# Kernel optimization log

Measured on AMD Instinct MI355X. Metric: run time of the kernel, lower is better.

## Reference

```python
import jax, jax.numpy as jnp
import numpy as np

BETA = 0.5

def setup_inputs() -> dict:
    key = jax.random.key(0)
    ks = jax.random.split(key, 12)
    B, H, d, hid = 2048, 100, 128, 256
    item_num, region_num, dist_num = 100000, 1000, 16
    return {
        "history": jax.random.randint(ks[0], (B, H), 0, item_num),
        "target": jax.random.randint(ks[1], (B,), 0, item_num),
        "history_region": jax.random.randint(ks[2], (B, H), 0, region_num),
        "target_region": jax.random.randint(ks[3], (B,), 0, region_num),
        "target_distance": jax.random.uniform(ks[4], (B,), dtype=jnp.float32),
        "E_hist": jax.random.normal(ks[5], (item_num, d), dtype=jnp.float32) * 0.01,
        "E_tgt": jax.random.normal(ks[6], (item_num, d), dtype=jnp.float32) * 0.01,
        "E_reg": jax.random.normal(ks[7], (region_num, d), dtype=jnp.float32) * 0.01,
        "E_dist": jax.random.normal(ks[8], (dist_num, d), dtype=jnp.float32) * 0.01,
        "W1": jax.random.normal(ks[9], (hid, 2 * d), dtype=jnp.float32) * 0.05,
        "b1": jnp.zeros((hid,), dtype=jnp.float32),
        "w2": jax.random.normal(ks[10], (hid,), dtype=jnp.float32) * 0.05,
    }

def reference(history, target, history_region, target_region, target_distance,
              E_hist, E_tgt, E_reg, E_dist, W1, b1, w2):
    # history embeddings: [B,H,2d]
    hist = jnp.concatenate([E_hist[history], E_reg[history_region]], axis=-1)
    # target embeddings: [B,1,2d]
    tgt = jnp.concatenate([E_tgt[target], E_reg[target_region]], axis=-1)[:, None, :]
    x = hist * tgt                                   # [B,H,2d]
    a = jax.nn.relu(jnp.einsum('bhd,kd->bhk', x, W1) + b1)  # [B,H,hid]
    score = jnp.einsum('bhk,k->bh', a, w2)           # [B,H]
    # distance bias: scalar per batch element
    dist = jnp.sum(target_distance[:, None] * E_dist[0], axis=1)  # [B]
    exp_A = jnp.exp(score + dist[:, None])           # [B,H]
    mask = (history != target[:, None]).astype(exp_A.dtype)
    exp_A = exp_A * mask
    exp_sum = jnp.power(jnp.sum(exp_A, axis=-1), BETA)  # [B]
    attn = exp_A / exp_sum[:, None]                  # [B,H]
    # weighted inner product: sum_h sum_d attn*hist*tgt
    pred = jnp.sum(hist * attn[:, :, None] * tgt, axis=(1, 2))  # [B]
    return jax.nn.sigmoid(pred)
```

## Files before the change

### kernel.cpp

```cpp
#include <hip/hip_runtime.h>
#include <stdint.h>

typedef __attribute__((ext_vector_type(8))) short bf16x8;
typedef __attribute__((ext_vector_type(4))) float f32x4;

#define HH  100
#define DD  128
#define HID 256

__device__ __forceinline__ unsigned short f2bf(float f) {
    unsigned int u = __float_as_uint(f);
    u += 0x7fffu + ((u >> 16) & 1u);
    return (unsigned short)(u >> 16);
}

__global__ void w1_pack(const float* __restrict__ W1, unsigned short* __restrict__ W1p) {
    int unit = blockIdx.x * 256 + threadIdx.x;
    int lane = unit & 63;
    int s    = (unit >> 6) & 7;
    int st   = unit >> 9;
    int col  = lane & 15, quad = lane >> 4;
    const float* src = W1 + (size_t)(st * 16 + col) * HID + s * 32 + quad * 8;
    union { unsigned short u[8]; bf16x8 v; } o;
    #pragma unroll
    for (int j = 0; j < 8; j++) o.u[j] = f2bf(src[j]);
    *(bf16x8*)(W1p + (size_t)unit * 8) = o.v;
}

__global__ __launch_bounds__(512, 4) void nais_kernel(
    const int* __restrict__ history,
    const int* __restrict__ target,
    const int* __restrict__ history_region,
    const int* __restrict__ target_region,
    const float* __restrict__ target_distance,
    const float* __restrict__ E_hist,
    const float* __restrict__ E_tgt,
    const float* __restrict__ E_reg,
    const float* __restrict__ E_dist,
    const float* __restrict__ b1,
    const float* __restrict__ w2,
    const unsigned short* __restrict__ W1p,
    float* __restrict__ out)
{
    __shared__ __align__(16) unsigned short As[7 * 4096];
    __shared__ __align__(16) float scorep[8][112];
    __shared__ __align__(16) float tgts[HID];
    __shared__ __align__(16) float b1s[HID];
    __shared__ __align__(16) float w2s[HID];
    __shared__ float xsum[112];
    __shared__ float eA[HH];
    __shared__ float exs[HH];
    __shared__ int hidx[HH];
    __shared__ int hreg[HH];
    __shared__ float s_sumE;

    const int b    = blockIdx.x;
    const int t    = threadIdx.x;
    const int lane = t & 63;
    const int wave = t >> 6;
    const int col  = lane & 15;
    const int quad = lane >> 4;

    const int   tg    = target[b];
    const float tdist = target_distance[b];

    if (t < HH) {
        hidx[t] = history[b * HH + t];
        hreg[t] = history_region[b * HH + t];
    }
    if (wave == 4) {
        float4 v;
        if (lane < 32) v = *(const float4*)(E_tgt + (size_t)tg * DD + lane * 4);
        else           v = *(const float4*)(E_reg + (size_t)target_region[b] * DD + (lane - 32) * 4);
        *(float4*)(tgts + lane * 4) = v;
    }
    if (wave == 5) {
        *(float4*)(b1s + lane * 4) = *(const float4*)(b1 + lane * 4);
        *(float4*)(w2s + lane * 4) = *(const float4*)(w2 + lane * 4);
    }
    if (wave == 6) {
        float v = E_dist[lane] + E_dist[64 + lane];
        #pragma unroll
        for (int off = 32; off; off >>= 1) v += __shfl_xor(v, off);
        if (lane == 0) s_sumE = v;
    }
    __syncthreads();

    if (wave < 7) {
        const int row = wave * 16 + col;
        const int rc  = (row < HH) ? row : row - 64;
        const int ih  = hidx[rc];
        const int ir  = hreg[rc];
        const float* ph = E_hist + (size_t)ih * DD + quad * 8;
        const float* pr = E_reg  + (size_t)ir * DD + quad * 8;
        unsigned short* ap = As + (size_t)wave * 4096;
        float acc = 0.f;
        #pragma unroll
        for (int s = 0; s < 8; s++) {
            const float* src = (s < 4) ? (ph + s * 32) : (pr + (s - 4) * 32);
            float4 v0 = *(const float4*)src;
            float4 v1 = *(const float4*)(src + 4);
            const float* tp = tgts + s * 32 + quad * 8;
            float4 t0 = *(const float4*)tp, t1 = *(const float4*)(tp + 4);
            float x0 = v0.x * t0.x, x1 = v0.y * t0.y, x2 = v0.z * t0.z, x3 = v0.w * t0.w;
            float x4 = v1.x * t1.x, x5 = v1.y * t1.y, x6 = v1.z * t1.z, x7 = v1.w * t1.w;
            acc += (x0 + x1) + (x2 + x3) + ((x4 + x5) + (x6 + x7));
            union { unsigned short u[8]; bf16x8 v; } fb;
            fb.u[0] = f2bf(x0); fb.u[1] = f2bf(x1); fb.u[2] = f2bf(x2); fb.u[3] = f2bf(x3);
            fb.u[4] = f2bf(x4); fb.u[5] = f2bf(x5); fb.u[6] = f2bf(x6); fb.u[7] = f2bf(x7);
            *(bf16x8*)(ap + (size_t)(s * 64 + lane) * 8) = fb.v;
        }
        float v = acc;
        v += __shfl_xor(v, 16);
        v += __shfl_xor(v, 32);
        if (quad == 0) xsum[row] = v;
    }

    bf16x8 w1f[16];
    #pragma unroll
    for (int i = 0; i < 16; i++) {
        const int unit = ((2 * wave + (i >> 3)) * 8 + (i & 7)) * 64 + lane;
        w1f[i] = *(const bf16x8*)(W1p + (size_t)unit * 8);
    }
    #pragma unroll
    for (int i = 0; i < 16; i++) asm volatile("" : "+v"(w1f[i]));
    __syncthreads();

    const int st0 = 2 * wave;
    const f32x4 bb0 = *(const f32x4*)&b1s[st0 * 16 + quad * 4];
    const f32x4 bb1 = *(const f32x4*)&b1s[st0 * 16 + 16 + quad * 4];
    const f32x4 ww0 = *(const f32x4*)&w2s[st0 * 16 + quad * 4];
    const f32x4 ww1 = *(const f32x4*)&w2s[st0 * 16 + 16 + quad * 4];
    #pragma unroll 1
    for (int i = 0; i < 7; i++) {
        int mt = wave + i; if (mt >= 7) mt -= 7;
        const unsigned short* ap = As + (size_t)mt * 4096;
        f32x4 a0 = {0.f, 0.f, 0.f, 0.f}, a1 = {0.f, 0.f, 0.f, 0.f};
        #pragma unroll
        for (int s = 0; s < 8; s++) {
            bf16x8 xf = *(const bf16x8*)(ap + (size_t)(s * 64 + lane) * 8);
            a0 = __builtin_amdgcn_mfma_f32_16x16x32_bf16(w1f[s],     xf, a0, 0, 0, 0);
            a1 = __builtin_amdgcn_mfma_f32_16x16x32_bf16(w1f[8 + s], xf, a1, 0, 0, 0);
        }
        float sp = 0.f;
        #pragma unroll
        for (int r = 0; r < 4; r++) {
            float z0 = a0[r] + bb0[r];
            float z1 = a1[r] + bb1[r];
            sp += ((z0 > 0.f) ? z0 * ww0[r] : 0.f) + ((z1 > 0.f) ? z1 * ww1[r] : 0.f);
        }
        sp += __shfl_xor(sp, 16);
        sp += __shfl_xor(sp, 32);
        if (quad == 0) scorep[wave][mt * 16 + col] = sp;
    }
    __syncthreads();

    float sc = 0.f;
    if (t < 112) {
        #pragma unroll
        for (int w = 0; w < 8; w++) sc += scorep[w][t];
    }
    const float dist = tdist * s_sumE;
    if (t < HH) {
        float e = (hidx[t] != tg) ? expf(sc + dist) : 0.f;
        eA[t]  = e;
        exs[t] = e * xsum[t];
    }
    __syncthreads();
    if (t < 64) {
        float s1 = eA[t]  + ((t + 64 < HH) ? eA[t + 64]  : 0.f);
        float s2 = exs[t] + ((t + 64 < HH) ? exs[t + 64] : 0.f);
        #pragma unroll
        for (int off = 32; off; off >>= 1) {
            s1 += __shfl_xor(s1, off);
            s2 += __shfl_xor(s2, off);
        }
        if (t == 0) {
            float pred = s2 / sqrtf(s1);
            out[b] = 1.f / (1.f + expf(-pred));
        }
    }
}

extern "C" void kernel_launch(void* const* d_in, const int* in_sizes, int n_in,
                              void* d_out, int out_size, void* d_ws, size_t ws_size,
                              hipStream_t stream) {
    const int*   history         = (const int*)d_in[0];
    const int*   target          = (const int*)d_in[1];
    const int*   history_region  = (const int*)d_in[2];
    const int*   target_region   = (const int*)d_in[3];
    const float* target_distance = (const float*)d_in[4];
    const float* E_hist          = (const float*)d_in[5];
    const float* E_tgt           = (const float*)d_in[6];
    const float* E_reg           = (const float*)d_in[7];
    const float* E_dist          = (const float*)d_in[8];
    const float* W1              = (const float*)d_in[9];
    const float* b1              = (const float*)d_in[10];
    const float* w2              = (const float*)d_in[11];

    unsigned short* W1p = (unsigned short*)d_ws;
    const int B = in_sizes[1];

    w1_pack<<<32, 256, 0, stream>>>(W1, W1p);
    nais_kernel<<<B, 512, 0, stream>>>(history, target, history_region, target_region,
                                       target_distance, E_hist, E_tgt, E_reg, E_dist,
                                       b1, w2, W1p, (float*)d_out);
}
```

Baseline: 178.2 us.

## Make blocks persistent over several batch rows with double-buffered gather/MFMA pipeline

```diff
diff --git a/kernel.cpp b/kernel.cpp
--- a/kernel.cpp
+++ b/kernel.cpp
@@ -7,6 +7,7 @@
 #define HH  100
 #define DD  128
 #define HID 256
+#define NT  7
 
 __device__ __forceinline__ unsigned short f2bf(float f) {
     unsigned int u = __float_as_uint(f);
@@ -27,7 +28,76 @@
     *(bf16x8*)(W1p + (size_t)unit * 8) = o.v;
 }
 
-__global__ __launch_bounds__(512, 4) void nais_kernel(
+__device__ __forceinline__ unsigned int cvt_pk_bf16(float lo, float hi) {
+    unsigned int r;
+    asm("v_cvt_pk_bf16_f32 %0, %1, %2" : "=v"(r) : "v"(lo), "v"(hi));
+    return r;
+}
+
+#define CONSUME(V0, V1, S, AP, TGT, ACC) do {                                     \
+    const float* tp_ = (TGT) + (S) * 32 + quad * 8;                               \
+    float4 t0_ = *(const float4*)tp_, t1_ = *(const float4*)(tp_ + 4);            \
+    float x0=(V0).x*t0_.x, x1=(V0).y*t0_.y, x2=(V0).z*t0_.z, x3=(V0).w*t0_.w;     \
+    float x4=(V1).x*t1_.x, x5=(V1).y*t1_.y, x6=(V1).z*t1_.z, x7=(V1).w*t1_.w;     \
+    (ACC) += (x0+x1)+(x2+x3)+((x4+x5)+(x6+x7));                                   \
+    union { unsigned int u[4]; int4 v; } fb_;                                     \
+    fb_.u[0]=cvt_pk_bf16(x0,x1); fb_.u[1]=cvt_pk_bf16(x2,x3);                     \
+    fb_.u[2]=cvt_pk_bf16(x4,x5); fb_.u[3]=cvt_pk_bf16(x6,x7);                     \
+    *(int4*)((AP) + (size_t)((S) * 64 + lane) * 8) = fb_.v;                       \
+} while (0)
+
+#define MFMA_PAIR(MM0, MM1) do {                                                  \
+    int m0_ = (MM0); if (m0_ >= NT) m0_ -= NT;                                    \
+    int m1_ = (MM1); if (m1_ >= NT) m1_ -= NT;                                    \
+    const unsigned short* a0p_ = Ab + m0_ * 4096;                                 \
+    const unsigned short* a1p_ = Ab + m1_ * 4096;                                 \
+    f32x4 c00_={0,0,0,0}, c01_={0,0,0,0}, c10_={0,0,0,0}, c11_={0,0,0,0};         \
+    _Pragma("unroll")                                                             \
+    for (int s_ = 0; s_ < 8; s_++) {                                              \
+        bf16x8 x0_ = *(const bf16x8*)(a0p_ + (size_t)(s_ * 64 + lane) * 8);       \
+        bf16x8 x1_ = *(const bf16x8*)(a1p_ + (size_t)(s_ * 64 + lane) * 8);       \
+        c00_ = __builtin_amdgcn_mfma_f32_16x16x32_bf16(w1f[s_],     x0_, c00_, 0,0,0); \
+        c01_ = __builtin_amdgcn_mfma_f32_16x16x32_bf16(w1f[8 + s_], x0_, c01_, 0,0,0); \
+        c10_ = __builtin_amdgcn_mfma_f32_16x16x32_bf16(w1f[s_],     x1_, c10_, 0,0,0); \
+        c11_ = __builtin_amdgcn_mfma_f32_16x16x32_bf16(w1f[8 + s_], x1_, c11_, 0,0,0); \
+    }                                                                             \
+    float sp0_ = 0.f, sp1_ = 0.f;                                                 \
+    _Pragma("unroll")                                                             \
+    for (int r_ = 0; r_ < 4; r_++) {                                              \
+        float z00_=c00_[r_]+bb0[r_], z01_=c01_[r_]+bb1[r_];                       \
+        float z10_=c10_[r_]+bb0[r_], z11_=c11_[r_]+bb1[r_];                       \
+        sp0_ += ((z00_>0.f)?z00_*ww0[r_]:0.f) + ((z01_>0.f)?z01_*ww1[r_]:0.f);    \
+        sp1_ += ((z10_>0.f)?z10_*ww0[r_]:0.f) + ((z11_>0.f)?z11_*ww1[r_]:0.f);    \
+    }                                                                             \
+    sp0_ += __shfl_xor(sp0_, 16); sp0_ += __shfl_xor(sp0_, 32);                   \
+    sp1_ += __shfl_xor(sp1_, 16); sp1_ += __shfl_xor(sp1_, 32);                   \
+    if (quad == 0) {                                                              \
+        scorep[wave][m0_ * 16 + col] = sp0_;                                      \
+        scorep[wave][m1_ * 16 + col] = sp1_;                                      \
+    }                                                                             \
+} while (0)
+
+#define MFMA_SINGLE(MM0) do {                                                     \
+    int m0_ = (MM0); if (m0_ >= NT) m0_ -= NT;                                    \
+    const unsigned short* a0p_ = Ab + m0_ * 4096;                                 \
+    f32x4 c00_={0,0,0,0}, c01_={0,0,0,0};                                         \
+    _Pragma("unroll")                                                             \
+    for (int s_ = 0; s_ < 8; s_++) {                                              \
+        bf16x8 x0_ = *(const bf16x8*)(a0p_ + (size_t)(s_ * 64 + lane) * 8);       \
+        c00_ = __builtin_amdgcn_mfma_f32_16x16x32_bf16(w1f[s_],     x0_, c00_, 0,0,0); \
+        c01_ = __builtin_amdgcn_mfma_f32_16x16x32_bf16(w1f[8 + s_], x0_, c01_, 0,0,0); \
+    }                                                                             \
+    float sp0_ = 0.f;                                                             \
+    _Pragma("unroll")                                                             \
+    for (int r_ = 0; r_ < 4; r_++) {                                              \
+        float z00_=c00_[r_]+bb0[r_], z01_=c01_[r_]+bb1[r_];                       \
+        sp0_ += ((z00_>0.f)?z00_*ww0[r_]:0.f) + ((z01_>0.f)?z01_*ww1[r_]:0.f);    \
+    }                                                                             \
+    sp0_ += __shfl_xor(sp0_, 16); sp0_ += __shfl_xor(sp0_, 32);                   \
+    if (quad == 0) scorep[wave][m0_ * 16 + col] = sp0_;                           \
+} while (0)
+
+__global__ __launch_bounds__(512, 2) void nais_kernel(
     const int* __restrict__ history,
     const int* __restrict__ target,
     const int* __restrict__ history_region,
@@ -40,81 +110,51 @@
     const float* __restrict__ b1,
     const float* __restrict__ w2,
     const unsigned short* __restrict__ W1p,
-    float* __restrict__ out)
+    float* __restrict__ out,
+    int Btot)
 {
-    __shared__ __align__(16) unsigned short As[7 * 4096];
-    __shared__ __align__(16) float scorep[8][112];
-    __shared__ __align__(16) float tgts[HID];
+    __shared__ __align__(16) unsigned short As[2][NT * 4096];
+    __shared__ __align__(16) float tgts3[3][HID];
     __shared__ __align__(16) float b1s[HID];
     __shared__ __align__(16) float w2s[HID];
-    __shared__ float xsum[112];
-    __shared__ float eA[HH];
-    __shared__ float exs[HH];
-    __shared__ int hidx[HH];
-    __shared__ int hreg[HH];
+    __shared__ __align__(16) int   hidx3[3][HH];
+    __shared__ __align__(16) int   hreg3[3][HH];
+    __shared__ __align__(16) float scorep[8][112];
+    __shared__ __align__(16) float xsum2[2][112];
+    __shared__ int   tgA[64];
+    __shared__ int   trA[64];
+    __shared__ float tdA[64];
+    __shared__ float p12[2][4];
     __shared__ float s_sumE;
 
-    const int b    = blockIdx.x;
     const int t    = threadIdx.x;
     const int lane = t & 63;
     const int wave = t >> 6;
     const int col  = lane & 15;
     const int quad = lane >> 4;
 
-    const int   tg    = target[b];
-    const float tdist = target_distance[b];
-
-    if (t < HH) {
-        hidx[t] = history[b * HH + t];
-        hreg[t] = history_region[b * HH + t];
+    const int NB   = (Btot + gridDim.x - 1) / gridDim.x;
+    const int base = blockIdx.x * NB;
+    int cnt = Btot - base;
+    if (cnt <= 0) return;
+    if (cnt > NB) cnt = NB;
+
+    if (t < cnt) {
+        tgA[t] = target[base + t];
+        trA[t] = target_region[base + t];
+        tdA[t] = target_distance[base + t];
     }
     if (wave == 4) {
-        float4 v;
-        if (lane < 32) v = *(const float4*)(E_tgt + (size_t)tg * DD + lane * 4);
-        else           v = *(const float4*)(E_reg + (size_t)target_region[b] * DD + (lane - 32) * 4);
-        *(float4*)(tgts + lane * 4) = v;
-    }
-    if (wave == 5) {
         *(float4*)(b1s + lane * 4) = *(const float4*)(b1 + lane * 4);
         *(float4*)(w2s + lane * 4) = *(const float4*)(w2 + lane * 4);
     }
-    if (wave == 6) {
+    if (wave == 5) {
         float v = E_dist[lane] + E_dist[64 + lane];
         #pragma unroll
         for (int off = 32; off; off >>= 1) v += __shfl_xor(v, off);
         if (lane == 0) s_sumE = v;
     }
     __syncthreads();
-
-    if (wave < 7) {
-        const int row = wave * 16 + col;
-        const int rc  = (row < HH) ? row : row - 64;
-        const int ih  = hidx[rc];
-        const int ir  = hreg[rc];
-        const float* ph = E_hist + (size_t)ih * DD + quad * 8;
-        const float* pr = E_reg  + (size_t)ir * DD + quad * 8;
-        unsigned short* ap = As + (size_t)wave * 4096;
-        float acc = 0.f;
-        #pragma unroll
-        for (int s = 0; s < 8; s++) {
-            const float* src = (s < 4) ? (ph + s * 32) : (pr + (s - 4) * 32);
-            float4 v0 = *(const float4*)src;
-            float4 v1 = *(const float4*)(src + 4);
-            const float* tp = tgts + s * 32 + quad * 8;
-            float4 t0 = *(const float4*)tp, t1 = *(const float4*)(tp + 4);
-            float x0 = v0.x * t0.x, x1 = v0.y * t0.y, x2 = v0.z * t0.z, x3 = v0.w * t0.w;
-            float x4 = v1.x * t1.x, x5 = v1.y * t1.y, x6 = v1.z * t1.z, x7 = v1.w * t1.w;
-            acc += (x0 + x1) + (x2 + x3) + ((x4 + x5) + (x6 + x7));
-            union { unsigned short u[8]; bf16x8 v; } fb;
-            fb.u[0] = f2bf(x0); fb.u[1] = f2bf(x1); fb.u[2] = f2bf(x2); fb.u[3] = f2bf(x3);
-            fb.u[4] = f2bf(x4); fb.u[5] = f2bf(x5); fb.u[6] = f2bf(x6); fb.u[7] = f2bf(x7);
-            *(bf16x8*)(ap + (size_t)(s * 64 + lane) * 8) = fb.v;
-        }
-        float v = acc;
-        v += __shfl_xor(v, 16);
-        v += __shfl_xor(v, 32);
-        if (quad == 0) xsum[row] = v;
-    }
 
     bf16x8 w1f[16];
     #pragma unroll
@@ -124,61 +164,161 @@
     }
     #pragma unroll
     for (int i = 0; i < 16; i++) asm volatile("" : "+v"(w1f[i]));
+
+    if (wave < 2 && wave < cnt) {
+        const int em = base + wave;
+        int4 mh = {0,0,0,0}, mr = {0,0,0,0};
+        if (lane < 25)      mh = *(const int4*)(history + (size_t)em * HH + lane * 4);
+        else if (lane < 50) mr = *(const int4*)(history_region + (size_t)em * HH + (lane - 25) * 4);
+        const int tg2 = tgA[wave], tr2 = trA[wave];
+        const float* tp2 = (lane < 32) ? (E_tgt + (size_t)tg2 * DD + lane * 4)
+                                       : (E_reg + (size_t)tr2 * DD + (lane - 32) * 4);
+        float4 mt4 = *(const float4*)tp2;
+        if (lane < 25)      *(int4*)&hidx3[wave][lane * 4] = mh;
+        else if (lane < 50) *(int4*)&hreg3[wave][(lane - 25) * 4] = mr;
+        *(float4*)&tgts3[wave][lane * 4] = mt4;
+    }
     __syncthreads();
+
+    if (wave < NT) {
+        const int row0 = wave * 16 + col;
+        const int rc  = (row0 < HH) ? row0 : row0 - 64;
+        const int ih  = hidx3[0][rc];
+        const int ir  = hreg3[0][rc];
+        const float* ph = E_hist + (size_t)ih * DD + quad * 8;
+        const float* pr = E_reg  + (size_t)ir * DD + quad * 8;
+        unsigned short* ap = &As[0][wave * 4096];
+        float4 g[16];
+        #pragma unroll
+        for (int s = 0; s < 4; s++) {
+            g[2*s]     = *(const float4*)(ph + s * 32);
+            g[2*s + 1] = *(const float4*)(ph + s * 32 + 4);
+            g[8 + 2*s] = *(const float4*)(pr + s * 32);
+            g[9 + 2*s] = *(const float4*)(pr + s * 32 + 4);
+        }
+        float acc = 0.f;
+        #pragma unroll
+        for (int s = 0; s < 8; s++) CONSUME(g[2*s], g[2*s+1], s, ap, tgts3[0], acc);
+        float v = acc;
+        v += __shfl_xor(v, 16);
+        v += __shfl_xor(v, 32);
+        if (quad == 0) xsum2[0][row0] = v;
+    }
 
     const int st0 = 2 * wave;
     const f32x4 bb0 = *(const f32x4*)&b1s[st0 * 16 + quad * 4];
     const f32x4 bb1 = *(const f32x4*)&b1s[st0 * 16 + 16 + quad * 4];
     const f32x4 ww0 = *(const f32x4*)&w2s[st0 * 16 + quad * 4];
     const f32x4 ww1 = *(const f32x4*)&w2s[st0 * 16 + 16 + quad * 4];
+
+    __syncthreads();
+
+    int cur = 0, cm = 0, nm = 1, n2 = 2;
+
     #pragma unroll 1
-    for (int i = 0; i < 7; i++) {
-        int mt = wave + i; if (mt >= 7) mt -= 7;
-        const unsigned short* ap = As + (size_t)mt * 4096;
-        f32x4 a0 = {0.f, 0.f, 0.f, 0.f}, a1 = {0.f, 0.f, 0.f, 0.f};
-        #pragma unroll
-        for (int s = 0; s < 8; s++) {
-            bf16x8 xf = *(const bf16x8*)(ap + (size_t)(s * 64 + lane) * 8);
-            a0 = __builtin_amdgcn_mfma_f32_16x16x32_bf16(w1f[s],     xf, a0, 0, 0, 0);
-            a1 = __builtin_amdgcn_mfma_f32_16x16x32_bf16(w1f[8 + s], xf, a1, 0, 0, 0);
-        }
-        float sp = 0.f;
-        #pragma unroll
-        for (int r = 0; r < 4; r++) {
-            float z0 = a0[r] + bb0[r];
-            float z1 = a1[r] + bb1[r];
-            sp += ((z0 > 0.f) ? z0 * ww0[r] : 0.f) + ((z1 > 0.f) ? z1 * ww1[r] : 0.f);
-        }
-        sp += __shfl_xor(sp, 16);
-        sp += __shfl_xor(sp, 32);
-        if (quad == 0) scorep[wave][mt * 16 + col] = sp;
-    }
-    __syncthreads();
-
-    float sc = 0.f;
-    if (t < 112) {
-        #pragma unroll
-        for (int w = 0; w < 8; w++) sc += scorep[w][t];
-    }
-    const float dist = tdist * s_sumE;
-    if (t < HH) {
-        float e = (hidx[t] != tg) ? expf(sc + dist) : 0.f;
-        eA[t]  = e;
-        exs[t] = e * xsum[t];
-    }
-    __syncthreads();
-    if (t < 64) {
-        float s1 = eA[t]  + ((t + 64 < HH) ? eA[t + 64]  : 0.f);
-        float s2 = exs[t] + ((t + 64 < HH) ? exs[t + 64] : 0.f);
-        #pragma unroll
-        for (int off = 32; off; off >>= 1) {
-            s1 += __shfl_xor(s1, off);
-            s2 += __shfl_xor(s2, off);
-        }
-        if (t == 0) {
-            float pred = s2 / sqrtf(s1);
-            out[b] = 1.f / (1.f + expf(-pred));
-        }
+    for (int i = 0; i < cnt; i++) {
+        const bool do_g = (i + 1 < cnt) && (wave < NT);
+        const bool do_m = (i + 2 < cnt) && (wave == 7);
+
+        float4 g[16];
+        int row0 = 0;
+        if (do_g) {
+            row0 = wave * 16 + col;
+            const int rc = (row0 < HH) ? row0 : row0 - 64;
+            const int ih = hidx3[nm][rc];
+            const int ir = hreg3[nm][rc];
+            const float* ph = E_hist + (size_t)ih * DD + quad * 8;
+            const float* pr = E_reg  + (size_t)ir * DD + quad * 8;
+            #pragma unroll
+            for (int s = 0; s < 4; s++) {
+                g[2*s]     = *(const float4*)(ph + s * 32);
+                g[2*s + 1] = *(const float4*)(ph + s * 32 + 4);
+                g[8 + 2*s] = *(const float4*)(pr + s * 32);
+                g[9 + 2*s] = *(const float4*)(pr + s * 32 + 4);
+            }
+        }
+        int4 mh = {0,0,0,0}, mr4 = {0,0,0,0};
+        float4 mt4 = {0.f, 0.f, 0.f, 0.f};
+        if (do_m) {
+            const int em = base + i + 2;
+            if (lane < 25)      mh  = *(const int4*)(history + (size_t)em * HH + lane * 4);
+            else if (lane < 50) mr4 = *(const int4*)(history_region + (size_t)em * HH + (lane - 25) * 4);
+            const int tg2 = tgA[i + 2], tr2 = trA[i + 2];
+            const float* tp2 = (lane < 32) ? (E_tgt + (size_t)tg2 * DD + lane * 4)
+                                           : (E_reg + (size_t)tr2 * DD + (lane - 32) * 4);
+            mt4 = *(const float4*)tp2;
+        }
+
+        const unsigned short* Ab = &As[cur][0];
+
+        MFMA_PAIR(wave,     wave + 1);
+        MFMA_PAIR(wave + 2, wave + 3);
+        MFMA_PAIR(wave + 4, wave + 5);
+        MFMA_SINGLE(wave + 6);
+
+        __syncthreads();
+
+        {
+            float sc = 0.f;
+            if (t < 112) {
+                #pragma unroll
+                for (int w = 0; w < 8; w++) sc += scorep[w][t];
+            }
+            float e1v = 0.f, e2v = 0.f;
+            if (t < HH) {
+                const float dist = tdA[i] * s_sumE;
+                if (hidx3[cm][t] != tgA[i]) {
+                    float e = expf(sc + dist);
+                    e1v = e;
+                    e2v = e * xsum2[cur][t];
+                }
+            }
+            if (wave < 2) {
+                #pragma unroll
+                for (int off = 32; off; off >>= 1) {
+                    e1v += __shfl_xor(e1v, off);
+                    e2v += __shfl_xor(e2v, off);
+                }
+                if (lane == 0) {
+                    p12[cur][wave]     = e1v;
+                    p12[cur][2 + wave] = e2v;
+                }
+            }
+            if (i > 0 && t == 128) {
+                float s1 = p12[cur ^ 1][0] + p12[cur ^ 1][1];
+                float s2 = p12[cur ^ 1][2] + p12[cur ^ 1][3];
+                float pred = s2 / sqrtf(s1);
+                out[base + i - 1] = 1.f / (1.f + expf(-pred));
+            }
+        }
+
+        if (do_g) {
+            unsigned short* An = &As[cur ^ 1][wave * 4096];
+            const float* tgt = &tgts3[nm][0];
+            float acc = 0.f;
+            #pragma unroll
+            for (int s = 0; s < 8; s++) CONSUME(g[2*s], g[2*s+1], s, An, tgt, acc);
+            float v = acc;
+            v += __shfl_xor(v, 16);
+            v += __shfl_xor(v, 32);
+            if (quad == 0) xsum2[cur ^ 1][row0] = v;
+        } else if (do_m) {
+            if (lane < 25)      *(int4*)&hidx3[n2][lane * 4] = mh;
+            else if (lane < 50) *(int4*)&hreg3[n2][(lane - 25) * 4] = mr4;
+            *(float4*)&tgts3[n2][lane * 4] = mt4;
+        }
+
+        __syncthreads();
+        cur ^= 1;
+        const int tmp = cm; cm = nm; nm = n2; n2 = tmp;
+    }
+
+    if (t == 0) {
+        const int sl = (cnt - 1) & 1;
+        float s1 = p12[sl][0] + p12[sl][1];
+        float s2 = p12[sl][2] + p12[sl][3];
+        float pred = s2 / sqrtf(s1);
+        out[base + cnt - 1] = 1.f / (1.f + expf(-pred));
     }
 }
 
@@ -201,8 +341,11 @@
     unsigned short* W1p = (unsigned short*)d_ws;
     const int B = in_sizes[1];
 
+    int grid = (B + 7) / 8;
+    if (grid > 256) grid = 256;
+
     w1_pack<<<32, 256, 0, stream>>>(W1, W1p);
-    nais_kernel<<<B, 512, 0, stream>>>(history, target, history_region, target_region,
-                                       target_distance, E_hist, E_tgt, E_reg, E_dist,
-                                       b1, w2, W1p, (float*)d_out);
-}
+    nais_kernel<<<grid, 512, 0, stream>>>(history, target, history_region, target_region,
+                                          target_distance, E_hist, E_tgt, E_reg, E_dist,
+                                          b1, w2, W1p, (float*)d_out, B);
+}
```

Result: slower. 185.8 us (+4.2%).

## Halve block to 4 waves, each owning 64 hidden units with batched gathers

Applied to the files above, without the earlier changes.

```diff
diff --git a/kernel.cpp b/kernel.cpp
--- a/kernel.cpp
+++ b/kernel.cpp
@@ -7,6 +7,7 @@
 #define HH  100
 #define DD  128
 #define HID 256
+#define NT  7
 
 __device__ __forceinline__ unsigned short f2bf(float f) {
     unsigned int u = __float_as_uint(f);
@@ -27,7 +28,25 @@
     *(bf16x8*)(W1p + (size_t)unit * 8) = o.v;
 }
 
-__global__ __launch_bounds__(512, 4) void nais_kernel(
+__device__ __forceinline__ unsigned int cvt_pk_bf16(float lo, float hi) {
+    unsigned int r;
+    asm("v_cvt_pk_bf16_f32 %0, %1, %2" : "=v"(r) : "v"(lo), "v"(hi));
+    return r;
+}
+
+#define CONSUME(V0, V1, S, AP, TGT, ACC) do {                                     \
+    const float* tp_ = (TGT) + (S) * 32 + quad * 8;                               \
+    float4 t0_ = *(const float4*)tp_, t1_ = *(const float4*)(tp_ + 4);            \
+    float x0=(V0).x*t0_.x, x1=(V0).y*t0_.y, x2=(V0).z*t0_.z, x3=(V0).w*t0_.w;     \
+    float x4=(V1).x*t1_.x, x5=(V1).y*t1_.y, x6=(V1).z*t1_.z, x7=(V1).w*t1_.w;     \
+    (ACC) += (x0+x1)+(x2+x3)+((x4+x5)+(x6+x7));                                   \
+    union { unsigned int u[4]; int4 v; } fb_;                                     \
+    fb_.u[0]=cvt_pk_bf16(x0,x1); fb_.u[1]=cvt_pk_bf16(x2,x3);                     \
+    fb_.u[2]=cvt_pk_bf16(x4,x5); fb_.u[3]=cvt_pk_bf16(x6,x7);                     \
+    *(int4*)((AP) + (size_t)((S) * 64 + lane) * 8) = fb_.v;                       \
+} while (0)
+
+__global__ __launch_bounds__(256, 2) void nais_kernel(
     const int* __restrict__ history,
     const int* __restrict__ target,
     const int* __restrict__ history_region,
@@ -42,12 +61,12 @@
     const unsigned short* __restrict__ W1p,
     float* __restrict__ out)
 {
-    __shared__ __align__(16) unsigned short As[7 * 4096];
-    __shared__ __align__(16) float scorep[8][112];
+    __shared__ __align__(16) unsigned short As[NT * 4096];
     __shared__ __align__(16) float tgts[HID];
     __shared__ __align__(16) float b1s[HID];
     __shared__ __align__(16) float w2s[HID];
-    __shared__ float xsum[112];
+    __shared__ __align__(16) float scorep[4][112];
+    __shared__ __align__(16) float xsum[112];
     __shared__ float eA[HH];
     __shared__ float exs[HH];
     __shared__ int hidx[HH];
@@ -68,17 +87,17 @@
         hidx[t] = history[b * HH + t];
         hreg[t] = history_region[b * HH + t];
     }
-    if (wave == 4) {
+    if (wave == 2) {
         float4 v;
         if (lane < 32) v = *(const float4*)(E_tgt + (size_t)tg * DD + lane * 4);
         else           v = *(const float4*)(E_reg + (size_t)target_region[b] * DD + (lane - 32) * 4);
         *(float4*)(tgts + lane * 4) = v;
     }
-    if (wave == 5) {
+    if (wave == 3) {
         *(float4*)(b1s + lane * 4) = *(const float4*)(b1 + lane * 4);
         *(float4*)(w2s + lane * 4) = *(const float4*)(w2 + lane * 4);
     }
-    if (wave == 6) {
+    if (wave == 1) {
         float v = E_dist[lane] + E_dist[64 + lane];
         #pragma unroll
         for (int off = 32; off; off >>= 1) v += __shfl_xor(v, off);
@@ -86,68 +105,74 @@
     }
     __syncthreads();
 
-    if (wave < 7) {
-        const int row = wave * 16 + col;
+    bf16x8 w1f[32];
+    #pragma unroll
+    for (int j = 0; j < 32; j++) {
+        const int unit = ((wave * 4 + (j >> 3)) * 8 + (j & 7)) * 64 + lane;
+        w1f[j] = *(const bf16x8*)(W1p + (size_t)unit * 8);
+    }
+    #pragma unroll
+    for (int j = 0; j < 32; j++) asm volatile("" : "+v"(w1f[j]));
+
+    #pragma unroll 1
+    for (int ti = 0; ti < 2; ti++) {
+        const int tile = wave + ti * 4;
+        if (tile >= NT) break;
+        const int row = tile * 16 + col;
         const int rc  = (row < HH) ? row : row - 64;
         const int ih  = hidx[rc];
         const int ir  = hreg[rc];
         const float* ph = E_hist + (size_t)ih * DD + quad * 8;
         const float* pr = E_reg  + (size_t)ir * DD + quad * 8;
-        unsigned short* ap = As + (size_t)wave * 4096;
+        unsigned short* ap = &As[tile * 4096];
+        float4 g[16];
+        #pragma unroll
+        for (int s = 0; s < 4; s++) {
+            g[2*s]     = *(const float4*)(ph + s * 32);
+            g[2*s + 1] = *(const float4*)(ph + s * 32 + 4);
+            g[8 + 2*s] = *(const float4*)(pr + s * 32);
+            g[9 + 2*s] = *(const float4*)(pr + s * 32 + 4);
+        }
         float acc = 0.f;
         #pragma unroll
-        for (int s = 0; s < 8; s++) {
-            const float* src = (s < 4) ? (ph + s * 32) : (pr + (s - 4) * 32);
-            float4 v0 = *(const float4*)src;
-            float4 v1 = *(const float4*)(src + 4);
-            const float* tp = tgts + s * 32 + quad * 8;
-            float4 t0 = *(const float4*)tp, t1 = *(const float4*)(tp + 4);
-            float x0 = v0.x * t0.x, x1 = v0.y * t0.y, x2 = v0.z * t0.z, x3 = v0.w * t0.w;
-            float x4 = v1.x * t1.x, x5 = v1.y * t1.y, x6 = v1.z * t1.z, x7 = v1.w * t1.w;
-            acc += (x0 + x1) + (x2 + x3) + ((x4 + x5) + (x6 + x7));
-            union { unsigned short u[8]; bf16x8 v; } fb;
-            fb.u[0] = f2bf(x0); fb.u[1] = f2bf(x1); fb.u[2] = f2bf(x2); fb.u[3] = f2bf(x3);
-            fb.u[4] = f2bf(x4); fb.u[5] = f2bf(x5); fb.u[6] = f2bf(x6); fb.u[7] = f2bf(x7);
-            *(bf16x8*)(ap + (size_t)(s * 64 + lane) * 8) = fb.v;
-        }
+        for (int s = 0; s < 8; s++) CONSUME(g[2*s], g[2*s+1], s, ap, tgts, acc);
         float v = acc;
         v += __shfl_xor(v, 16);
         v += __shfl_xor(v, 32);
         if (quad == 0) xsum[row] = v;
     }
 
-    bf16x8 w1f[16];
-    #pragma unroll
-    for (int i = 0; i < 16; i++) {
-        const int unit = ((2 * wave + (i >> 3)) * 8 + (i & 7)) * 64 + lane;
-        w1f[i] = *(const bf16x8*)(W1p + (size_t)unit * 8);
-    }
-    #pragma unroll
-    for (int i = 0; i < 16; i++) asm volatile("" : "+v"(w1f[i]));
-    __syncthreads();
-
-    const int st0 = 2 * wave;
-    const f32x4 bb0 = *(const f32x4*)&b1s[st0 * 16 + quad * 4];
-    const f32x4 bb1 = *(const f32x4*)&b1s[st0 * 16 + 16 + quad * 4];
-    const f32x4 ww0 = *(const f32x4*)&w2s[st0 * 16 + quad * 4];
-    const f32x4 ww1 = *(const f32x4*)&w2s[st0 * 16 + 16 + quad * 4];
+    f32x4 bbv[4], wwv[4];
+    #pragma unroll
+    for (int st = 0; st < 4; st++) {
+        bbv[st] = *(const f32x4*)&b1s[(wave * 4 + st) * 16 + quad * 4];
+        wwv[st] = *(const f32x4*)&w2s[(wave * 4 + st) * 16 + quad * 4];
+    }
+
+    __syncthreads();
+
     #pragma unroll 1
-    for (int i = 0; i < 7; i++) {
-        int mt = wave + i; if (mt >= 7) mt -= 7;
-        const unsigned short* ap = As + (size_t)mt * 4096;
-        f32x4 a0 = {0.f, 0.f, 0.f, 0.f}, a1 = {0.f, 0.f, 0.f, 0.f};
+    for (int i = 0; i < NT; i++) {
+        int mt = wave * 2 + i; if (mt >= NT) mt -= NT;
+        const unsigned short* ap = &As[mt * 4096];
+        f32x4 c0 = {0,0,0,0}, c1 = {0,0,0,0}, c2 = {0,0,0,0}, c3 = {0,0,0,0};
         #pragma unroll
         for (int s = 0; s < 8; s++) {
             bf16x8 xf = *(const bf16x8*)(ap + (size_t)(s * 64 + lane) * 8);
-            a0 = __builtin_amdgcn_mfma_f32_16x16x32_bf16(w1f[s],     xf, a0, 0, 0, 0);
-            a1 = __builtin_amdgcn_mfma_f32_16x16x32_bf16(w1f[8 + s], xf, a1, 0, 0, 0);
+            c0 = __builtin_amdgcn_mfma_f32_16x16x32_bf16(w1f[s],      xf, c0, 0, 0, 0);
+            c1 = __builtin_amdgcn_mfma_f32_16x16x32_bf16(w1f[8 + s],  xf, c1, 0, 0, 0);
+            c2 = __builtin_amdgcn_mfma_f32_16x16x32_bf16(w1f[16 + s], xf, c2, 0, 0, 0);
+            c3 = __builtin_amdgcn_mfma_f32_16x16x32_bf16(w1f[24 + s], xf, c3, 0, 0, 0);
         }
         float sp = 0.f;
         #pragma unroll
         for (int r = 0; r < 4; r++) {
-            float z0 = a0[r] + bb0[r];
-            float z1 = a1[r] + bb1[r];
-            sp += ((z0 > 0.f) ? z0 * ww0[r] : 0.f) + ((z1 > 0.f) ? z1 * ww1[r] : 0.f);
+            float z0 = c0[r] + bbv[0][r];
+            float z1 = c1[r] + bbv[1][r];
+            float z2 = c2[r] + bbv[2][r];
+            float z3 = c3[r] + bbv[3][r];
+            sp += ((z0 > 0.f) ? z0 * wwv[0][r] : 0.f) + ((z1 > 0.f) ? z1 * wwv[1][r] : 0.f)
+                + ((z2 > 0.f) ? z2 * wwv[2][r] : 0.f) + ((z3 > 0.f) ? z3 * wwv[3][r] : 0.f);
         }
         sp += __shfl_xor(sp, 16);
         sp += __shfl_xor(sp, 32);
@@ -158,7 +183,7 @@
     float sc = 0.f;
     if (t < 112) {
         #pragma unroll
-        for (int w = 0; w < 8; w++) sc += scorep[w][t];
+        for (int w = 0; w < 4; w++) sc += scorep[w][t];
     }
     const float dist = tdist * s_sumE;
     if (t < HH) {
@@ -202,7 +227,7 @@
     const int B = in_sizes[1];
 
     w1_pack<<<32, 256, 0, stream>>>(W1, W1p);
-    nais_kernel<<<B, 512, 0, stream>>>(history, target, history_region, target_region,
+    nais_kernel<<<B, 256, 0, stream>>>(history, target, history_region, target_region,
                                        target_distance, E_hist, E_tgt, E_reg, E_dist,
                                        b1, w2, W1p, (float*)d_out);
 }
```

Result: no change. 178.9 us (+0.4%).
